# Performance work log

Hardware: AMD Instinct MI355X
Metric: run time of the kernel (lower is better)

The kernel has to match this reference:

```python
import jax, jax.numpy as jnp
import numpy as np

N_NODES = 4_194_304
N_GRAPHS = 65_536

# Orthonormal (Frobenius) basis for symmetric traceless 3x3 matrices: the
# real l=2 components of 1o x 1o -> 2e (Clebsch-Gordan up to basis choice).
_s2 = 1.0 / np.sqrt(2.0)
_B = np.zeros((5, 3, 3), dtype=np.float32)
_B[0, 0, 1] = _B[0, 1, 0] = _s2            # xy
_B[1, 1, 2] = _B[1, 2, 1] = _s2            # yz
_B[2, 0, 2] = _B[2, 2, 0] = _s2            # xz
_B[3, 0, 0] = _s2; _B[3, 1, 1] = -_s2      # x^2 - y^2
_B[4, 0, 0] = _B[4, 1, 1] = -1.0 / np.sqrt(6.0); _B[4, 2, 2] = 2.0 / np.sqrt(6.0)
B_CG = jnp.asarray(_B)

INV_SQRT2 = 0.7071067811865476
INV_SQRT3 = 0.5773502691896258


def setup_inputs() -> dict:
    key = jax.random.key(0)
    k1, k2, k3, k4, k5, k6 = jax.random.split(key, 6)
    z = jax.random.randint(k1, (N_NODES,), 0, 100, dtype=jnp.int32)
    pos = jax.random.normal(k2, (N_NODES, 3), dtype=jnp.float32)
    batch = jnp.sort(jax.random.randint(k3, (N_NODES,), 0, N_GRAPHS, dtype=jnp.int32))
    # FullyConnectedTensorProduct weights: 5 paths, mul pattern (1,1,mul_out)
    # 0e*0e->2x0e (2) + 1o*1o->2x0e (2) + 0e*1o->2x1o (2) + 1o*0e->2x1o (2) + 1o*1o->1x2e (1) = 9
    w_tp = jax.random.normal(k4, (9,), dtype=jnp.float32)
    fc_w = jax.random.normal(k5, (1, 13), dtype=jnp.float32) / np.sqrt(13.0)
    fc_b = jax.random.normal(k6, (1,), dtype=jnp.float32) * 0.01
    return {"z": z, "pos": pos, "batch": batch, "w_tp": w_tp, "fc_w": fc_w, "fc_b": fc_b}


def reference(z, pos, batch, w_tp, fc_w, fc_b):
    s = z.astype(jnp.float32)                      # [N] scalar (0e) part
    v = pos                                        # [N,3] vector (1o) part
    wA, wB = w_tp[0:2], w_tp[2:4]                  # -> 2x0e paths
    wC, wD = w_tp[4:6], w_tp[6:8]                  # -> 2x1o paths
    wE = w_tp[8]                                   # -> 1x2e path

    # CG tensor product x (x) x -> 2x0e + 2x1o + 1x2e, path-normalized by 1/sqrt(#paths)
    ss = s * s                                     # 0e x 0e -> 0e
    dot = jnp.sum(v * v, axis=-1)                  # 1o . 1o -> 0e (CG = delta/sqrt3)
    out0 = (ss[:, None] * wA + (dot * INV_SQRT3)[:, None] * wB) * INV_SQRT2   # [N,2]
    sv = s[:, None] * v                            # 0e x 1o -> 1o
    out1 = (sv[:, None, :] * (wC + wD)[None, :, None]) * INV_SQRT2            # [N,2,3]
    quad = jnp.einsum('kij,ni,nj->nk', B_CG, v, v) # 1o x 1o -> 2e            # [N,5]
    out2 = wE * quad

    x = jnp.concatenate([out0, out1.reshape(-1, 6), out2], axis=-1)  # [N,13]
    x = jax.nn.relu(x)                             # (as in source: relu on all irreps)
    y = x @ fc_w.T + fc_b                          # [N,1] -> 1x0e
    y = jnp.tanh(y)                                # Gate on pure scalars = scalar act

    sums = jax.ops.segment_sum(y, batch, num_segments=N_GRAPHS)                # [G,1]
    counts = jax.ops.segment_sum(jnp.ones((batch.shape[0], 1), y.dtype), batch,
                                 num_segments=N_GRAPHS)
    return sums / jnp.maximum(counts, 1.0)
```

## Files before the change

kernel.cpp:

```cpp
#include <hip/hip_runtime.h>

static constexpr float INV_SQRT2 = 0.70710678118654752f;
static constexpr float INV_SQRT3 = 0.57735026918962576f;
static constexpr float SQRT2     = 1.41421356237309505f;
static constexpr float INV_SQRT6 = 0.40824829046386302f;

static constexpr int W_GRAPHS = 8;

__global__ __launch_bounds__(256) void find_bounds(
    const int* __restrict__ batch,
    int*       __restrict__ bnd,
    int n, int n_graphs)
{
    const int i = blockIdx.x * blockDim.x + threadIdx.x;
    if (i >= n) return;
    const int cur  = batch[i];
    const int prev = (i == 0) ? -1 : batch[i - 1];
    for (int g = prev + 1; g <= cur; ++g) bnd[g] = i;
    if (i == n - 1) {
        for (int g = cur + 1; g <= n_graphs; ++g) bnd[g] = n;
    }
}

__global__ __launch_bounds__(256) void e3nn_g8(
    const int*   __restrict__ z,
    const float* __restrict__ pos,
    const int*   __restrict__ bnd,
    const float* __restrict__ w_tp,
    const float* __restrict__ fc_w,
    const float* __restrict__ fc_b,
    float*       __restrict__ out,
    int n_graphs)
{
    const int lane = threadIdx.x & 63;
    const int wave = (blockIdx.x * blockDim.x + threadIdx.x) >> 6;
    const int g0   = wave * W_GRAPHS;
    if (g0 >= n_graphs) return;

    const float wA0 = w_tp[0], wA1 = w_tp[1];
    const float wB0 = w_tp[2], wB1 = w_tp[3];
    const float c0  = (w_tp[4] + w_tp[6]) * INV_SQRT2;
    const float c1  = (w_tp[5] + w_tp[7]) * INV_SQRT2;
    const float wE  = w_tp[8];
    float fw[13];
#pragma unroll
    for (int j = 0; j < 13; ++j) fw[j] = fc_w[j];
    const float fb = fc_b[0];

    int bval = 0;
    {
        const int idx = g0 + lane;
        if (lane <= W_GRAPHS && idx <= n_graphs) bval = bnd[idx];
    }
    const int nb = __shfl_down(bval, 1);
    const int B0 = __shfl(bval, 0), B1 = __shfl(bval, 1);
    const int B2 = __shfl(bval, 2), B3 = __shfl(bval, 3);
    const int B4 = __shfl(bval, 4), B5 = __shfl(bval, 5);
    const int B6 = __shfl(bval, 6), B7 = __shfl(bval, 7);
    const int B8 = __shfl(bval, 8);

    float a0 = 0.f, a1 = 0.f, a2 = 0.f, a3 = 0.f;
    float a4 = 0.f, a5 = 0.f, a6 = 0.f, a7 = 0.f;

#pragma unroll 1
    for (int base = B0; base < B8; base += 64) {
        const int i = base + lane;
        if (i < B8) {
            const float sc = (float)z[i];
            const float v0 = pos[i * 3 + 0];
            const float v1 = pos[i * 3 + 1];
            const float v2 = pos[i * 3 + 2];

            const float ss   = sc * sc;
            const float dot3 = (v0 * v0 + v1 * v1 + v2 * v2) * INV_SQRT3;

            const float x0 = (ss * wA0 + dot3 * wB0) * INV_SQRT2;
            const float x1 = (ss * wA1 + dot3 * wB1) * INV_SQRT2;

            const float sv0 = sc * v0, sv1 = sc * v1, sv2 = sc * v2;
            const float x2 = sv0 * c0, x3 = sv1 * c0, x4 = sv2 * c0;
            const float x5 = sv0 * c1, x6 = sv1 * c1, x7 = sv2 * c1;

            const float x8  = wE * (SQRT2 * v0 * v1);
            const float x9  = wE * (SQRT2 * v1 * v2);
            const float x10 = wE * (SQRT2 * v0 * v2);
            const float x11 = wE * (INV_SQRT2 * (v0 * v0 - v1 * v1));
            const float x12 = wE * (INV_SQRT6 * (2.f * v2 * v2 - v0 * v0 - v1 * v1));

            float acc = fb;
            acc += fmaxf(x0,  0.f) * fw[0];
            acc += fmaxf(x1,  0.f) * fw[1];
            acc += fmaxf(x2,  0.f) * fw[2];
            acc += fmaxf(x3,  0.f) * fw[3];
            acc += fmaxf(x4,  0.f) * fw[4];
            acc += fmaxf(x5,  0.f) * fw[5];
            acc += fmaxf(x6,  0.f) * fw[6];
            acc += fmaxf(x7,  0.f) * fw[7];
            acc += fmaxf(x8,  0.f) * fw[8];
            acc += fmaxf(x9,  0.f) * fw[9];
            acc += fmaxf(x10, 0.f) * fw[10];
            acc += fmaxf(x11, 0.f) * fw[11];
            acc += fmaxf(x12, 0.f) * fw[12];
            const float y = tanhf(acc);

            const int gi = (i >= B1) + (i >= B2) + (i >= B3) + (i >= B4)
                         + (i >= B5) + (i >= B6) + (i >= B7);
            a0 += (gi == 0) ? y : 0.f;
            a1 += (gi == 1) ? y : 0.f;
            a2 += (gi == 2) ? y : 0.f;
            a3 += (gi == 3) ? y : 0.f;
            a4 += (gi == 4) ? y : 0.f;
            a5 += (gi == 5) ? y : 0.f;
            a6 += (gi == 6) ? y : 0.f;
            a7 += (gi == 7) ? y : 0.f;
        }
    }

#pragma unroll
    for (int off = 32; off >= 1; off >>= 1) {
        a0 += __shfl_xor(a0, off);
        a1 += __shfl_xor(a1, off);
        a2 += __shfl_xor(a2, off);
        a3 += __shfl_xor(a3, off);
        a4 += __shfl_xor(a4, off);
        a5 += __shfl_xor(a5, off);
        a6 += __shfl_xor(a6, off);
        a7 += __shfl_xor(a7, off);
    }

    if (lane < W_GRAPHS && g0 + lane < n_graphs) {
        float sel = (lane == 0) ? a0
                  : (lane == 1) ? a1
                  : (lane == 2) ? a2
                  : (lane == 3) ? a3
                  : (lane == 4) ? a4
                  : (lane == 5) ? a5
                  : (lane == 6) ? a6
                  :               a7;
        const float c = (float)(nb - bval);
        out[g0 + lane] = sel / fmaxf(c, 1.0f);
    }
}

extern "C" void kernel_launch(void* const* d_in, const int* in_sizes, int n_in,
                              void* d_out, int out_size, void* d_ws, size_t ws_size,
                              hipStream_t stream) {
    const int*   z     = (const int*)d_in[0];
    const float* pos   = (const float*)d_in[1];
    const int*   batch = (const int*)d_in[2];
    const float* w_tp  = (const float*)d_in[3];
    const float* fc_w  = (const float*)d_in[4];
    const float* fc_b  = (const float*)d_in[5];

    float* out = (float*)d_out;
    int*   bnd = (int*)d_ws;
    const int n        = in_sizes[0];
    const int n_graphs = out_size;

    const int b1 = (n + 255) / 256;
    find_bounds<<<b1, 256, 0, stream>>>(batch, bnd, n, n_graphs);

    const int waves = (n_graphs + W_GRAPHS - 1) / W_GRAPHS;
    const int b2    = (waves * 64 + 255) / 256;
    e3nn_g8<<<b2, 256, 0, stream>>>(z, pos, bnd, w_tp, fc_w, fc_b,
                                    out, n_graphs);
}
```

Before: 32.32 us.

## Replace bounds-finding kernel with per-wave binary search over sorted batch

Removes the separate find_bounds pass, which read the whole batch array and wrote a boundary table. Instead, each wave's first nine lanes binary-search the sorted batch array to find their graph boundaries, and everything runs in a single fused kernel. This avoids one full pass over the 16 MB batch array plus a kernel launch. In exchange it adds about 22 dependent, scattered global loads per wave before the main loop can start.

```diff
diff --git a/kernel.cpp b/kernel.cpp
--- a/kernel.cpp
+++ b/kernel.cpp
@@ -7,30 +7,15 @@
 
 static constexpr int W_GRAPHS = 8;
 
-__global__ __launch_bounds__(256) void find_bounds(
-    const int* __restrict__ batch,
-    int*       __restrict__ bnd,
-    int n, int n_graphs)
-{
-    const int i = blockIdx.x * blockDim.x + threadIdx.x;
-    if (i >= n) return;
-    const int cur  = batch[i];
-    const int prev = (i == 0) ? -1 : batch[i - 1];
-    for (int g = prev + 1; g <= cur; ++g) bnd[g] = i;
-    if (i == n - 1) {
-        for (int g = cur + 1; g <= n_graphs; ++g) bnd[g] = n;
-    }
-}
-
-__global__ __launch_bounds__(256) void e3nn_g8(
+__global__ __launch_bounds__(256) void e3nn_fused(
     const int*   __restrict__ z,
     const float* __restrict__ pos,
-    const int*   __restrict__ bnd,
+    const int*   __restrict__ batch,
     const float* __restrict__ w_tp,
     const float* __restrict__ fc_w,
     const float* __restrict__ fc_b,
     float*       __restrict__ out,
-    int n_graphs)
+    int n, int n_graphs)
 {
     const int lane = threadIdx.x & 63;
     const int wave = (blockIdx.x * blockDim.x + threadIdx.x) >> 6;
@@ -47,11 +32,16 @@
     for (int j = 0; j < 13; ++j) fw[j] = fc_w[j];
     const float fb = fc_b[0];
 
+    const int tl     = (lane < W_GRAPHS) ? lane : W_GRAPHS;
+    const int target = g0 + tl;
+    unsigned p2 = 1;
+    while (p2 < (unsigned)n) p2 <<= 1;
     int bval = 0;
-    {
-        const int idx = g0 + lane;
-        if (lane <= W_GRAPHS && idx <= n_graphs) bval = bnd[idx];
+    for (unsigned step = p2 >> 1; step > 0; step >>= 1) {
+        const unsigned cand = (unsigned)bval + step;
+        if (cand <= (unsigned)n && batch[cand - 1] < target) bval = (int)cand;
     }
+
     const int nb = __shfl_down(bval, 1);
     const int B0 = __shfl(bval, 0), B1 = __shfl(bval, 1);
     const int B2 = __shfl(bval, 2), B3 = __shfl(bval, 3);
@@ -153,15 +143,11 @@
     const float* fc_b  = (const float*)d_in[5];
 
     float* out = (float*)d_out;
-    int*   bnd = (int*)d_ws;
     const int n        = in_sizes[0];
     const int n_graphs = out_size;
 
-    const int b1 = (n + 255) / 256;
-    find_bounds<<<b1, 256, 0, stream>>>(batch, bnd, n, n_graphs);
-
     const int waves = (n_graphs + W_GRAPHS - 1) / W_GRAPHS;
-    const int b2    = (waves * 64 + 255) / 256;
-    e3nn_g8<<<b2, 256, 0, stream>>>(z, pos, bnd, w_tp, fc_w, fc_b,
-                                    out, n_graphs);
+    const int blocks = (waves * 64 + 255) / 256;
+    e3nn_fused<<<blocks, 256, 0, stream>>>(z, pos, batch, w_tp, fc_w, fc_b,
+                                           out, n, n_graphs);
 }
```

Result: no change. 31.80 us (-1.6%).
